# Kernel tuning notes

Measured on AMD Instinct MI355X. Metric: run time of the kernel, lower is better.

The kernel has to match this reference:

```python
import jax, jax.numpy as jnp
import numpy as np

N_NODES = 100_000
N_EDGES = 1_600_000
N_GRAPHS = 512
NF = 64        # n_node_feats
H1 = 128       # hidden width
H2 = 64        # dim_node_emb
DIM_OUT = 1
STEPS = 4      # set2set processing steps


def _lin(x, W, b):
    # torch Linear convention: y = x @ W.T + b, W: [out, in]
    return x @ W.T + b


def _gelu(x):
    return jax.nn.gelu(x, approximate=False)  # torch.nn.GELU default (erf)


def _lstm_cell(x, h, c, Wih, Whh, bih, bhh):
    g = x @ Wih.T + bih + h @ Whh.T + bhh
    i, f, gg, o = jnp.split(g, 4, axis=-1)  # torch gate order: i, f, g, o
    i, f, o = jax.nn.sigmoid(i), jax.nn.sigmoid(f), jax.nn.sigmoid(o)
    gg = jnp.tanh(gg)
    c = f * c + i * gg
    h = o * jnp.tanh(c)
    return h, c


def setup_inputs() -> dict:
    key = jax.random.key(0)
    ks = jax.random.split(key, 24)
    p = lambda k, shp: jax.random.normal(k, shp, dtype=jnp.float32) * 0.05
    inp = {
        "x": jax.random.normal(ks[0], (N_NODES, NF), dtype=jnp.float32),
        "edge_index": jax.random.randint(ks[1], (2, N_EDGES), 0, N_NODES, dtype=jnp.int32),
        "batch": jnp.sort(jax.random.randint(ks[2], (N_NODES,), 0, N_GRAPHS, dtype=jnp.int32)),
        "nfc_W": p(ks[3], (H1, NF)), "nfc_b": p(ks[4], (H1,)),
        "gc1_W": p(ks[5], (H1, H1)), "gc1_b": p(ks[6], (H1,)),
        "gc2_W": p(ks[7], (H2, H1)), "gc2_b": p(ks[8], (H2,)),
        "lstm0_Wih": p(ks[9], (4 * H2, 2 * H2)), "lstm0_Whh": p(ks[10], (4 * H2, H2)),
        "lstm0_bih": p(ks[11], (4 * H2,)), "lstm0_bhh": p(ks[12], (4 * H2,)),
        "lstm1_Wih": p(ks[13], (4 * H2, H2)), "lstm1_Whh": p(ks[14], (4 * H2, H2)),
        "lstm1_bih": p(ks[15], (4 * H2,)), "lstm1_bhh": p(ks[16], (4 * H2,)),
        "fc1_W": p(ks[17], (32, 2 * H2)), "fc1_b": p(ks[18], (32,)),
        "fc2_W": p(ks[19], (DIM_OUT, 32)), "fc2_b": p(ks[20], (DIM_OUT,)),
    }
    return inp


def _forward(x, edge_index, batch, nfc_W, nfc_b, gc1_W, gc1_b, gc2_W, gc2_b,
             lstm0_Wih, lstm0_Whh, lstm0_bih, lstm0_bhh,
             lstm1_Wih, lstm1_Whh, lstm1_bih, lstm1_bhh,
             fc1_W, fc1_b, fc2_W, fc2_b):
    src, dst = edge_index[0], edge_index[1]

    def gin_conv(h, W, b):
        # PyG GINConv, eps=0: lin((1+eps)*x + sum_{j in N(i)} x_j)
        agg = jax.ops.segment_sum(h[src], dst, num_segments=N_NODES)
        return _lin(h + agg, W, b)

    h = _gelu(_lin(x, nfc_W, nfc_b))
    h = _gelu(gin_conv(h, gc1_W, gc1_b))
    h = _gelu(gin_conv(h, gc2_W, gc2_b))
    # F.normalize(p=2, dim=1)
    h = h / jnp.maximum(jnp.linalg.norm(h, axis=1, keepdims=True), 1e-12)

    # Set2Set: 2-layer LSTM, 4 processing steps, scatter-softmax attention
    B = N_GRAPHS
    h0 = jnp.zeros((B, H2), jnp.float32); c0 = jnp.zeros((B, H2), jnp.float32)
    h1 = jnp.zeros((B, H2), jnp.float32); c1 = jnp.zeros((B, H2), jnp.float32)
    q_star = jnp.zeros((B, 2 * H2), jnp.float32)
    for _ in range(STEPS):
        h0, c0 = _lstm_cell(q_star, h0, c0, lstm0_Wih, lstm0_Whh, lstm0_bih, lstm0_bhh)
        h1, c1 = _lstm_cell(h0, h1, c1, lstm1_Wih, lstm1_Whh, lstm1_bih, lstm1_bhh)
        q = h1  # [B, H2]
        e = jnp.sum(h * q[batch], axis=-1, keepdims=True)  # [N, 1]
        m = jax.ops.segment_max(e, batch, num_segments=B)
        ex = jnp.exp(e - m[batch])
        s = jax.ops.segment_sum(ex, batch, num_segments=B)
        a = ex / (s[batch] + 1e-16)
        r = jax.ops.segment_sum(a * h, batch, num_segments=B)  # [B, H2]
        q_star = jnp.concatenate([q, r], axis=-1)

    z = _gelu(_lin(q_star, fc1_W, fc1_b))
    z = _lin(z, fc2_W, fc2_b)
    return z, h


def reference(x, edge_index, batch, nfc_W, nfc_b, gc1_W, gc1_b, gc2_W, gc2_b,
              lstm0_Wih, lstm0_Whh, lstm0_bih, lstm0_bhh,
              lstm1_Wih, lstm1_Whh, lstm1_bih, lstm1_bhh,
              fc1_W, fc1_b, fc2_W, fc2_b):
    return _forward(x, edge_index, batch, nfc_W, nfc_b, gc1_W, gc1_b, gc2_W, gc2_b,
                    lstm0_Wih, lstm0_Whh, lstm0_bih, lstm0_bhh,
                    lstm1_Wih, lstm1_Whh, lstm1_bih, lstm1_bhh,
                    fc1_W, fc1_b, fc2_W, fc2_b)
```

## Files before the change

### kernel.cpp

```cpp
#include <hip/hip_runtime.h>
#include <hip/hip_bf16.h>
#include <hip/hip_fp16.h>
#include <math.h>

constexpr int N  = 100000;
constexpr int E  = 1600000;
constexpr int NG = 512;
constexpr int NF = 64;
constexpr int H1 = 128;
constexpr int H2 = 64;

constexpr int BW   = 128;
constexpr int NB   = (N + BW - 1) / BW;
constexpr int CAP  = 2600;
constexpr int CHUNK = 4096;

constexpr int MAXN = 416;
constexpr int RST  = 68;

typedef __attribute__((ext_vector_type(8))) short short8;
typedef __attribute__((ext_vector_type(4))) float f32x4;

__device__ __forceinline__ float gelu_f(float x) {
    return 0.5f * x * (1.0f + erff(x * 0.70710678118654752f));
}
__device__ __forceinline__ float sigmoid_f(float x) {
    return 1.0f / (1.0f + expf(-x));
}
__device__ __forceinline__ float waveAllSum(float v) {
    #pragma unroll
    for (int m = 32; m; m >>= 1) v += __shfl_xor(v, m);
    return v;
}
__device__ __forceinline__ unsigned short f2bf(float x) {
    __hip_bfloat16 b = __float2bfloat16(x);
    return *reinterpret_cast<unsigned short*>(&b);
}
__device__ __forceinline__ float bf2f(unsigned short u) {
    return __uint_as_float(((unsigned int)u) << 16);
}
__device__ __forceinline__ float bf_lo(unsigned int u) { return __uint_as_float(u << 16); }
__device__ __forceinline__ float bf_hi(unsigned int u) { return __uint_as_float(u & 0xffff0000u); }

__device__ __forceinline__ void bfsplit(float v, unsigned short& hi, unsigned short& lo) {
    hi = f2bf(v);
    lo = f2bf(v - bf2f(hi));
}

__global__ __launch_bounds__(256) void setup_kernel(const int* __restrict__ batch,
                                                    const float* __restrict__ Wih0, const float* __restrict__ Whh0,
                                                    const float* __restrict__ bih0, const float* __restrict__ bhh0,
                                                    const float* __restrict__ Wih1, const float* __restrict__ Whh1,
                                                    const float* __restrict__ bih1, const float* __restrict__ bhh1,
                                                    float* __restrict__ WT0, float* __restrict__ WT1,
                                                    float* __restrict__ b0, float* __restrict__ b1,
                                                    int* __restrict__ bcursor, int* __restrict__ gstart) {
    int i = blockIdx.x * 256 + threadIdx.x;
    if (i < 192 * 256) {
        int k = i >> 8, j = i & 255;
        WT0[i] = (k < 128) ? Wih0[j * 128 + k] : Whh0[j * 64 + (k - 128)];
    }
    if (i < 128 * 256) {
        int k = i >> 8, j = i & 255;
        WT1[i] = (k < 64) ? Wih1[j * 64 + k] : Whh1[j * 64 + (k - 64)];
    }
    if (i < 256) { b0[i] = bih0[i] + bhh0[i]; b1[i] = bih1[i] + bhh1[i]; }
    if (i < NB) bcursor[i] = i * CAP;
    if (i <= NG) {
        if (i == NG) gstart[NG] = N;
        else {
            int lo = 0, hi = N;
            while (lo < hi) {
                int mid = (lo + hi) >> 1;
                if (batch[mid] < i) lo = mid + 1; else hi = mid;
            }
            gstart[i] = lo;
        }
    }
}

__global__ __launch_bounds__(256) void bin_scatter_kernel(const int* __restrict__ ei,
                                                          int* __restrict__ bcursor,
                                                          int* __restrict__ pairs) {
    __shared__ int hist[NB];
    __shared__ int start_s[NB];
    __shared__ int lcur[NB];
    int tid = threadIdx.x;
    int e0 = blockIdx.x * CHUNK;
    for (int b = tid; b < NB; b += 256) hist[b] = 0;
    __syncthreads();
    #pragma unroll 4
    for (int k = 0; k < CHUNK / 256; ++k) {
        int e = e0 + k * 256 + tid;
        if (e < E) atomicAdd(&hist[ei[E + e] >> 7], 1);
    }
    __syncthreads();
    for (int b = tid; b < NB; b += 256) {
        if (hist[b]) start_s[b] = atomicAdd(&bcursor[b], hist[b]);
        lcur[b] = 0;
    }
    __syncthreads();
    #pragma unroll 4
    for (int k = 0; k < CHUNK / 256; ++k) {
        int e = e0 + k * 256 + tid;
        if (e < E) {
            int d = ei[E + e];
            int s = ei[e];
            int b = d >> 7;
            int pos = start_s[b] + atomicAdd(&lcur[b], 1);
            if (pos < (b + 1) * CAP) pairs[pos] = (s << 7) | (d & 127);
        }
    }
}

__global__ __launch_bounds__(256) void csr_bucket_kernel(const int* __restrict__ pairs,
                                                         const int* __restrict__ bcursor,
                                                         int* __restrict__ srcs,
                                                         int2* __restrict__ nrange) {
    __shared__ int cnt_l[BW];
    __shared__ int cur_l[BW];
    __shared__ int wt[2];
    int b = blockIdx.x;
    int tid = threadIdx.x;
    int base = b * CAP;
    int cnt = bcursor[b] - base;
    if (cnt > CAP) cnt = CAP;
    if (tid < BW) cnt_l[tid] = 0;
    __syncthreads();
    for (int i = tid; i < cnt; i += 256) {
        atomicAdd(&cnt_l[pairs[base + i] & 127], 1);
    }
    __syncthreads();
    if (tid < BW) {
        int v = cnt_l[tid];
        int lane = tid & 63, w = tid >> 6;
        int incl = v;
        #pragma unroll
        for (int off = 1; off < 64; off <<= 1) {
            int t = __shfl_up(incl, off);
            if (lane >= off) incl += t;
        }
        if (lane == 63) wt[w] = incl;
        __syncthreads();
        int excl = (w ? wt[0] : 0) + incl - v;
        int node = b * BW + tid;
        if (node < N) nrange[node] = make_int2(base + excl, base + excl + v);
        cur_l[tid] = excl;
    } else {
        __syncthreads();
    }
    __syncthreads();
    for (int i = tid; i < cnt; i += 256) {
        int p = pairs[base + i];
        int pos = atomicAdd(&cur_l[p & 127], 1);
        srcs[base + pos] = p >> 7;
    }
}

template <int ID, int OD>
__global__ __launch_bounds__(256) void lin_mfma_kernel(const float* __restrict__ in,
                                                       const float* __restrict__ W,
                                                       const float* __restrict__ bias,
                                                       unsigned short* __restrict__ out_bf, int nrows) {
    constexpr int KC = 32;
    constexpr int NCH = ID / KC;
    constexpr int AST = 40;
    constexpr int NCT = OD / 16;
    constexpr int LDSU = 2 * 128 * AST + 2 * OD * AST;
    __shared__ __align__(16) unsigned short lds[LDSU];
    unsigned short* Ahi = lds;
    unsigned short* Alo = lds + 128 * AST;
    unsigned short* Whi = lds + 2 * 128 * AST;
    unsigned short* Wlo = lds + 2 * 128 * AST + OD * AST;

    int tid = threadIdx.x;
    int w = tid >> 6, lane = tid & 63;
    int m15 = lane & 15, quad = lane >> 4;
    int nb = blockIdx.x * 128;

    f32x4 acc[2][NCT];
    #pragma unroll
    for (int rt = 0; rt < 2; ++rt)
        #pragma unroll
        for (int ct = 0; ct < NCT; ++ct) acc[rt][ct] = (f32x4)0.f;

    for (int c = 0; c < NCH; ++c) {
        int kb = c * KC;
        #pragma unroll
        for (int it = 0; it < 4; ++it) {
            int f4 = it * 256 + tid;
            int row = f4 >> 3, kq = (f4 & 7) * 4;
            float4 v = make_float4(0.f, 0.f, 0.f, 0.f);
            if (nb + row < nrows) v = *(const float4*)&in[(size_t)(nb + row) * ID + kb + kq];
            unsigned short h0, h1, h2, h3, l0, l1, l2, l3;
            bfsplit(v.x, h0, l0); bfsplit(v.y, h1, l1);
            bfsplit(v.z, h2, l2); bfsplit(v.w, h3, l3);
            uint2 uh, ul;
            uh.x = (unsigned int)h0 | ((unsigned int)h1 << 16);
            uh.y = (unsigned int)h2 | ((unsigned int)h3 << 16);
            ul.x = (unsigned int)l0 | ((unsigned int)l1 << 16);
            ul.y = (unsigned int)l2 | ((unsigned int)l3 << 16);
            *(uint2*)&Ahi[row * AST + kq] = uh;
            *(uint2*)&Alo[row * AST + kq] = ul;
        }
        #pragma unroll
        for (int it = 0; it < OD / 32; ++it) {
            int f4 = it * 256 + tid;
            int o = f4 >> 3, kq = (f4 & 7) * 4;
            float4 v = *(const float4*)&W[(size_t)o * ID + kb + kq];
            unsigned short h0, h1, h2, h3, l0, l1, l2, l3;
            bfsplit(v.x, h0, l0); bfsplit(v.y, h1, l1);
            bfsplit(v.z, h2, l2); bfsplit(v.w, h3, l3);
            uint2 uh, ul;
            uh.x = (unsigned int)h0 | ((unsigned int)h1 << 16);
            uh.y = (unsigned int)h2 | ((unsigned int)h3 << 16);
            ul.x = (unsigned int)l0 | ((unsigned int)l1 << 16);
            ul.y = (unsigned int)l2 | ((unsigned int)l3 << 16);
            *(uint2*)&Whi[o * AST + kq] = uh;
            *(uint2*)&Wlo[o * AST + kq] = ul;
        }
        __syncthreads();

        short8 ah0 = *(const short8*)&Ahi[(w * 32 + m15) * AST + quad * 8];
        short8 ah1 = *(const short8*)&Ahi[(w * 32 + 16 + m15) * AST + quad * 8];
        short8 al0 = *(const short8*)&Alo[(w * 32 + m15) * AST + quad * 8];
        short8 al1 = *(const short8*)&Alo[(w * 32 + 16 + m15) * AST + quad * 8];
        #pragma unroll
        for (int ct = 0; ct < NCT; ++ct) {
            short8 bh = *(const short8*)&Whi[(ct * 16 + m15) * AST + quad * 8];
            short8 bl = *(const short8*)&Wlo[(ct * 16 + m15) * AST + quad * 8];
            acc[0][ct] = __builtin_amdgcn_mfma_f32_16x16x32_bf16(ah0, bh, acc[0][ct], 0, 0, 0);
            acc[0][ct] = __builtin_amdgcn_mfma_f32_16x16x32_bf16(ah0, bl, acc[0][ct], 0, 0, 0);
            acc[0][ct] = __builtin_amdgcn_mfma_f32_16x16x32_bf16(al0, bh, acc[0][ct], 0, 0, 0);
            acc[1][ct] = __builtin_amdgcn_mfma_f32_16x16x32_bf16(ah1, bh, acc[1][ct], 0, 0, 0);
            acc[1][ct] = __builtin_amdgcn_mfma_f32_16x16x32_bf16(ah1, bl, acc[1][ct], 0, 0, 0);
            acc[1][ct] = __builtin_amdgcn_mfma_f32_16x16x32_bf16(al1, bh, acc[1][ct], 0, 0, 0);
        }
        __syncthreads();
    }

    float bcol[NCT];
    #pragma unroll
    for (int ct = 0; ct < NCT; ++ct) bcol[ct] = bias[ct * 16 + m15];

    constexpr int EPS = OD + 8;
    unsigned short* ep = lds;
    #pragma unroll
    for (int rt = 0; rt < 2; ++rt)
        #pragma unroll
        for (int ct = 0; ct < NCT; ++ct)
            #pragma unroll
            for (int r = 0; r < 4; ++r) {
                int rl = w * 32 + rt * 16 + quad * 4 + r;
                float v = gelu_f(acc[rt][ct][r] + bcol[ct]);
                ep[rl * EPS + ct * 16 + m15] = f2bf(v);
            }
    __syncthreads();
    constexpr int U4 = 128 * OD / 8;
    for (int i = tid; i < U4; i += 256) {
        int row = i / (OD / 8);
        int off = (i % (OD / 8)) * 8;
        int grow = nb + row;
        if (grow < nrows) {
            uint4 v = *(const uint4*)&ep[row * EPS + off];
            *(uint4*)(out_bf + (size_t)grow * OD + off) = v;
        }
    }
}

__global__ __launch_bounds__(256) void agg_kernel(const uint2* __restrict__ hb2,
                                                  const int2* __restrict__ nrange,
                                                  const int* __restrict__ srcs,
                                                  uint4* __restrict__ utab) {
    int wave = threadIdx.x >> 6, lane = threadIdx.x & 63;
    int half = lane >> 5, hl = lane & 31;
    int n = blockIdx.x * 4 + wave;
    if (n >= N) return;
    int2 rng = nrange[n];
    int s0 = rng.x, deg = rng.y - rng.x;
    int m1 = deg < 64 ? deg : 64;
    int pre = (lane < m1) ? srcs[s0 + lane] : 0;
    float a0 = 0.f, a1 = 0.f, a2 = 0.f, a3 = 0.f;
    int t = 0;
    for (; t + 8 <= m1; t += 8) {
        int i0 = __shfl(pre, t + half);
        int i1 = __shfl(pre, t + 2 + half);
        int i2 = __shfl(pre, t + 4 + half);
        int i3 = __shfl(pre, t + 6 + half);
        uint2 u0 = hb2[(size_t)i0 * 32 + hl];
        uint2 u1 = hb2[(size_t)i1 * 32 + hl];
        uint2 u2 = hb2[(size_t)i2 * 32 + hl];
        uint2 u3 = hb2[(size_t)i3 * 32 + hl];
        a0 += bf_lo(u0.x); a1 += bf_hi(u0.x); a2 += bf_lo(u0.y); a3 += bf_hi(u0.y);
        a0 += bf_lo(u1.x); a1 += bf_hi(u1.x); a2 += bf_lo(u1.y); a3 += bf_hi(u1.y);
        a0 += bf_lo(u2.x); a1 += bf_hi(u2.x); a2 += bf_lo(u2.y); a3 += bf_hi(u2.y);
        a0 += bf_lo(u3.x); a1 += bf_hi(u3.x); a2 += bf_lo(u3.y); a3 += bf_hi(u3.y);
    }
    for (; t < m1; t += 2) {
        int idx = t + half;
        int idc = idx < m1 ? idx : 0;
        int s = __shfl(pre, idc);
        if (idx < m1) {
            uint2 u = hb2[(size_t)s * 32 + hl];
            a0 += bf_lo(u.x); a1 += bf_hi(u.x); a2 += bf_lo(u.y); a3 += bf_hi(u.y);
        }
    }
    for (int j = 64 + half; j < deg; j += 2) {
        int s = srcs[s0 + j];
        uint2 u = hb2[(size_t)s * 32 + hl];
        a0 += bf_lo(u.x); a1 += bf_hi(u.x); a2 += bf_lo(u.y); a3 += bf_hi(u.y);
    }
    a0 += __shfl_down(a0, 32);
    a1 += __shfl_down(a1, 32);
    a2 += __shfl_down(a2, 32);
    a3 += __shfl_down(a3, 32);
    if (half == 0) {
        uint2 u = hb2[(size_t)n * 32 + hl];
        a0 += bf_lo(u.x); a1 += bf_hi(u.x); a2 += bf_lo(u.y); a3 += bf_hi(u.y);
        unsigned short h0, h1, h2, h3, l0, l1, l2, l3;
        bfsplit(a0, h0, l0); bfsplit(a1, h1, l1);
        bfsplit(a2, h2, l2); bfsplit(a3, h3, l3);
        uint4 o;
        o.x = (unsigned int)h0 | ((unsigned int)h1 << 16);
        o.y = (unsigned int)h2 | ((unsigned int)h3 << 16);
        o.z = (unsigned int)l0 | ((unsigned int)l1 << 16);
        o.w = (unsigned int)l2 | ((unsigned int)l3 << 16);
        utab[(size_t)n * 32 + hl] = o;
    }
}

__global__ __launch_bounds__(256) void lin2_fused_kernel(const uint4* __restrict__ in4,
                                                         const float* __restrict__ W1,
                                                         const float* __restrict__ b1,
                                                         const float* __restrict__ W2,
                                                         unsigned short* __restrict__ y2,
                                                         int nrows) {
    constexpr int AST = 40;
    __shared__ __align__(16) unsigned short lds[4 * 128 * AST];
    unsigned short* Ahi = lds;
    unsigned short* Alo = lds + 128 * AST;
    unsigned short* Whi = lds + 2 * 128 * AST;
    unsigned short* Wlo = lds + 3 * 128 * AST;

    int tid = threadIdx.x;
    int w = tid >> 6, lane = tid & 63;
    int m15 = lane & 15, quad = lane >> 4;
    int nb = blockIdx.x * 128;

    f32x4 acc[2][8];
    #pragma unroll
    for (int rt = 0; rt < 2; ++rt)
        #pragma unroll
        for (int ct = 0; ct < 8; ++ct) acc[rt][ct] = (f32x4)0.f;

    for (int c = 0; c < 4; ++c) {
        #pragma unroll
        for (int it = 0; it < 4; ++it) {
            int i = it * 256 + tid;
            int row = i >> 3, grp = i & 7;
            uint4 u = make_uint4(0u, 0u, 0u, 0u);
            if (nb + row < nrows) u = in4[(size_t)(nb + row) * 32 + c * 8 + grp];
            *(uint2*)&Ahi[row * AST + grp * 4] = make_uint2(u.x, u.y);
            *(uint2*)&Alo[row * AST + grp * 4] = make_uint2(u.z, u.w);
        }
        #pragma unroll
        for (int it = 0; it < 4; ++it) {
            int f4 = it * 256 + tid;
            int o = f4 >> 3, kq = (f4 & 7) * 4;
            float4 v = *(const float4*)&W1[(size_t)o * 128 + c * 32 + kq];
            unsigned short h0, h1, h2, h3, l0, l1, l2, l3;
            bfsplit(v.x, h0, l0); bfsplit(v.y, h1, l1);
            bfsplit(v.z, h2, l2); bfsplit(v.w, h3, l3);
            uint2 uh, ul;
            uh.x = (unsigned int)h0 | ((unsigned int)h1 << 16);
            uh.y = (unsigned int)h2 | ((unsigned int)h3 << 16);
            ul.x = (unsigned int)l0 | ((unsigned int)l1 << 16);
            ul.y = (unsigned int)l2 | ((unsigned int)l3 << 16);
            *(uint2*)&Whi[o * AST + kq] = uh;
            *(uint2*)&Wlo[o * AST + kq] = ul;
        }
        __syncthreads();
        short8 ah0 = *(const short8*)&Ahi[(w * 32 + m15) * AST + quad * 8];
        short8 ah1 = *(const short8*)&Ahi[(w * 32 + 16 + m15) * AST + quad * 8];
        short8 al0 = *(const short8*)&Alo[(w * 32 + m15) * AST + quad * 8];
        short8 al1 = *(const short8*)&Alo[(w * 32 + 16 + m15) * AST + quad * 8];
        #pragma unroll
        for (int ct = 0; ct < 8; ++ct) {
            short8 bh = *(const short8*)&Whi[(ct * 16 + m15) * AST + quad * 8];
            short8 bl = *(const short8*)&Wlo[(ct * 16 + m15) * AST + quad * 8];
            acc[0][ct] = __builtin_amdgcn_mfma_f32_16x16x32_bf16(ah0, bh, acc[0][ct], 0, 0, 0);
            acc[0][ct] = __builtin_amdgcn_mfma_f32_16x16x32_bf16(ah0, bl, acc[0][ct], 0, 0, 0);
            acc[0][ct] = __builtin_amdgcn_mfma_f32_16x16x32_bf16(al0, bh, acc[0][ct], 0, 0, 0);
            acc[1][ct] = __builtin_amdgcn_mfma_f32_16x16x32_bf16(ah1, bh, acc[1][ct], 0, 0, 0);
            acc[1][ct] = __builtin_amdgcn_mfma_f32_16x16x32_bf16(ah1, bl, acc[1][ct], 0, 0, 0);
            acc[1][ct] = __builtin_amdgcn_mfma_f32_16x16x32_bf16(al1, bh, acc[1][ct], 0, 0, 0);
        }
        __syncthreads();
    }

    #pragma unroll
    for (int ct = 0; ct < 8; ++ct) {
        float bc = b1[ct * 16 + m15];
        #pragma unroll
        for (int rt = 0; rt < 2; ++rt)
            #pragma unroll
            for (int r = 0; r < 4; ++r)
                acc[rt][ct][r] = gelu_f(acc[rt][ct][r] + bc);
    }

    f32x4 acc2[2][4];
    #pragma unroll
    for (int rt = 0; rt < 2; ++rt)
        #pragma unroll
        for (int ct = 0; ct < 4; ++ct) acc2[rt][ct] = (f32x4)0.f;

    for (int c2 = 0; c2 < 4; ++c2) {
        __syncthreads();
        #pragma unroll
        for (int rt = 0; rt < 2; ++rt)
            #pragma unroll
            for (int cc = 0; cc < 2; ++cc) {
                int ct = c2 * 2 + cc;
                #pragma unroll
                for (int r = 0; r < 4; ++r) {
                    int node = w * 32 + rt * 16 + quad * 4 + r;
                    unsigned short hi, lo;
                    bfsplit(acc[rt][ct][r], hi, lo);
                    Ahi[node * AST + cc * 16 + m15] = hi;
                    Alo[node * AST + cc * 16 + m15] = lo;
                }
            }
        #pragma unroll
        for (int it = 0; it < 2; ++it) {
            int f4 = it * 256 + tid;
            int o = f4 >> 3, kq = (f4 & 7) * 4;
            float4 v = *(const float4*)&W2[(size_t)o * 128 + c2 * 32 + kq];
            unsigned short h0, h1, h2, h3, l0, l1, l2, l3;
            bfsplit(v.x, h0, l0); bfsplit(v.y, h1, l1);
            bfsplit(v.z, h2, l2); bfsplit(v.w, h3, l3);
            uint2 uh, ul;
            uh.x = (unsigned int)h0 | ((unsigned int)h1 << 16);
            uh.y = (unsigned int)h2 | ((unsigned int)h3 << 16);
            ul.x = (unsigned int)l0 | ((unsigned int)l1 << 16);
            ul.y = (unsigned int)l2 | ((unsigned int)l3 << 16);
            *(uint2*)&Whi[o * AST + kq] = uh;
            *(uint2*)&Wlo[o * AST + kq] = ul;
        }
        __syncthreads();
        short8 ah0 = *(const short8*)&Ahi[(w * 32 + m15) * AST + quad * 8];
        short8 ah1 = *(const short8*)&Ahi[(w * 32 + 16 + m15) * AST + quad * 8];
        short8 al0 = *(const short8*)&Alo[(w * 32 + m15) * AST + quad * 8];
        short8 al1 = *(const short8*)&Alo[(w * 32 + 16 + m15) * AST + quad * 8];
        #pragma unroll
        for (int ct = 0; ct < 4; ++ct) {
            short8 bh = *(const short8*)&Whi[(ct * 16 + m15) * AST + quad * 8];
            short8 bl = *(const short8*)&Wlo[(ct * 16 + m15) * AST + quad * 8];
            acc2[0][ct] = __builtin_amdgcn_mfma_f32_16x16x32_bf16(ah0, bh, acc2[0][ct], 0, 0, 0);
            acc2[0][ct] = __builtin_amdgcn_mfma_f32_16x16x32_bf16(ah0, bl, acc2[0][ct], 0, 0, 0);
            acc2[0][ct] = __builtin_amdgcn_mfma_f32_16x16x32_bf16(al0, bh, acc2[0][ct], 0, 0, 0);
            acc2[1][ct] = __builtin_amdgcn_mfma_f32_16x16x32_bf16(ah1, bh, acc2[1][ct], 0, 0, 0);
            acc2[1][ct] = __builtin_amdgcn_mfma_f32_16x16x32_bf16(ah1, bl, acc2[1][ct], 0, 0, 0);
            acc2[1][ct] = __builtin_amdgcn_mfma_f32_16x16x32_bf16(al1, bh, acc2[1][ct], 0, 0, 0);
        }
    }
    __syncthreads();

    constexpr int EPS = 72;
    unsigned short* ep = lds;
    #pragma unroll
    for (int rt = 0; rt < 2; ++rt)
        #pragma unroll
        for (int ct = 0; ct < 4; ++ct)
            #pragma unroll
            for (int r = 0; r < 4; ++r) {
                int rl = w * 32 + rt * 16 + quad * 4 + r;
                __half hv = __float2half(acc2[rt][ct][r]);
                ep[rl * EPS + ct * 16 + m15] = *reinterpret_cast<unsigned short*>(&hv);
            }
    __syncthreads();
    for (int i = tid; i < 1024; i += 256) {
        int row = i >> 3, off = (i & 7) * 8;
        int grow = nb + row;
        if (grow < nrows)
            *(uint4*)(y2 + (size_t)grow * 64 + off) = *(const uint4*)&ep[row * EPS + off];
    }
}

__global__ __launch_bounds__(256) void agg2_norm_kernel(const uint2* __restrict__ y2,
                                                        const int2* __restrict__ nrange,
                                                        const int* __restrict__ srcs,
                                                        const float* __restrict__ b2,
                                                        float* __restrict__ hn) {
    int wave = threadIdx.x >> 6, lane = threadIdx.x & 63;
    int qw = lane >> 4, ql = lane & 15;
    int n = blockIdx.x * 4 + wave;
    if (n >= N) return;
    int2 rng = nrange[n];
    int s0 = rng.x, deg = rng.y - rng.x;
    int m1 = deg < 64 ? deg : 64;
    int pre = (lane < m1) ? srcs[s0 + lane] : 0;
    float a0 = 0.f, a1 = 0.f, a2 = 0.f, a3 = 0.f;
    auto addu = [&](uint2 u) {
        float2 f01 = __half22float2(*reinterpret_cast<__half2*>(&u.x));
        float2 f23 = __half22float2(*reinterpret_cast<__half2*>(&u.y));
        a0 += f01.x; a1 += f01.y; a2 += f23.x; a3 += f23.y;
    };
    int t = 0;
    for (; t + 8 <= m1; t += 8) {
        int i0 = __shfl(pre, t + qw);
        int i1 = __shfl(pre, t + 4 + qw);
        uint2 u0 = y2[(size_t)i0 * 16 + ql];
        uint2 u1 = y2[(size_t)i1 * 16 + ql];
        addu(u0); addu(u1);
    }
    for (; t < m1; t += 4) {
        int idx = t + qw;
        int s = __shfl(pre, idx < m1 ? idx : 0);
        if (idx < m1) addu(y2[(size_t)s * 16 + ql]);
    }
    for (int j = 64 + qw; j < deg; j += 4) addu(y2[(size_t)srcs[s0 + j] * 16 + ql]);
    a0 += __shfl_down(a0, 32); a1 += __shfl_down(a1, 32);
    a2 += __shfl_down(a2, 32); a3 += __shfl_down(a3, 32);
    a0 += __shfl_down(a0, 16); a1 += __shfl_down(a1, 16);
    a2 += __shfl_down(a2, 16); a3 += __shfl_down(a3, 16);
    if (qw == 0) {
        addu(y2[(size_t)n * 16 + ql]);
        float4 bv = *(const float4*)&b2[ql * 4];
        float v0 = gelu_f(a0 + bv.x), v1 = gelu_f(a1 + bv.y);
        float v2 = gelu_f(a2 + bv.z), v3 = gelu_f(a3 + bv.w);
        float ss = v0 * v0 + v1 * v1 + v2 * v2 + v3 * v3;
        #pragma unroll
        for (int mm = 1; mm < 16; mm <<= 1) ss += __shfl_xor(ss, mm);
        float d = fmaxf(sqrtf(ss), 1e-12f);
        *(float4*)&hn[(size_t)n * 64 + ql * 4] = make_float4(v0 / d, v1 / d, v2 / d, v3 / d);
    }
}

__global__ __launch_bounds__(256) void set2set_kernel(const float* __restrict__ hn,
                                                      const int* __restrict__ gstart,
                                                      const float* __restrict__ WT0, const float* __restrict__ b0,
                                                      const float* __restrict__ WT1, const float* __restrict__ b1,
                                                      float* __restrict__ qstar_out) {
    __shared__ __align__(16) unsigned short hL[MAXN * RST];
    __shared__ float av[MAXN];
    __shared__ __align__(16) float xc0[192];
    __shared__ __align__(16) float xc1[128];
    __shared__ __align__(16) float gates[256];
    __shared__ float c0v[H2], c1v[H2];
    __shared__ float red[4];
    __shared__ float rp[4][H2];
    __shared__ float sp[4];

    int g = blockIdx.x;
    int tid = threadIdx.x, w = tid >> 6, lane = tid & 63;
    int s0 = gstart[g], s1 = gstart[g + 1];
    int cnt = s1 - s0;
    int cL = cnt < MAXN ? cnt : MAXN;
    const float* hq = xc1 + 64;

    for (int idx = tid; idx < cL * 16; idx += 256) {
        int n = idx >> 4, p4 = idx & 15;
        float4 v = *(const float4*)&hn[(size_t)(s0 + n) * 64 + p4 * 4];
        uint2 u;
        u.x = (unsigned int)f2bf(v.x) | ((unsigned int)f2bf(v.y) << 16);
        u.y = (unsigned int)f2bf(v.z) | ((unsigned int)f2bf(v.w) << 16);
        *(uint2*)&hL[n * RST + p4 * 4] = u;
    }
    if (tid < 192) xc0[tid] = 0.f;
    if (tid < 128) xc1[tid] = 0.f;
    if (tid < H2) { c0v[tid] = 0.f; c1v[tid] = 0.f; }
    float b0v = b0[tid], b1v = b1[tid];
    __syncthreads();

    for (int step = 0; step < 4; ++step) {
        {
            float a0 = 0.f, a1 = 0.f, a2 = 0.f, a3 = 0.f;
            #pragma unroll 8
            for (int k = 0; k < 192; k += 4) {
                a0 += xc0[k]     * WT0[(k)     * 256 + tid];
                a1 += xc0[k + 1] * WT0[(k + 1) * 256 + tid];
                a2 += xc0[k + 2] * WT0[(k + 2) * 256 + tid];
                a3 += xc0[k + 3] * WT0[(k + 3) * 256 + tid];
            }
            gates[tid] = (a0 + a1) + (a2 + a3) + b0v;
        }
        __syncthreads();
        if (tid < H2) {
            float ii = sigmoid_f(gates[tid]), ff = sigmoid_f(gates[H2 + tid]);
            float gg = tanhf(gates[2 * H2 + tid]), oo = sigmoid_f(gates[3 * H2 + tid]);
            float c = ff * c0v[tid] + ii * gg;
            float h = oo * tanhf(c);
            c0v[tid] = c; xc0[128 + tid] = h; xc1[tid] = h;
        }
        __syncthreads();
        {
            float a0 = 0.f, a1 = 0.f, a2 = 0.f, a3 = 0.f;
            #pragma unroll 8
            for (int k = 0; k < 128; k += 4) {
                a0 += xc1[k]     * WT1[(k)     * 256 + tid];
                a1 += xc1[k + 1] * WT1[(k + 1) * 256 + tid];
                a2 += xc1[k + 2] * WT1[(k + 2) * 256 + tid];
                a3 += xc1[k + 3] * WT1[(k + 3) * 256 + tid];
            }
            gates[tid] = (a0 + a1) + (a2 + a3) + b1v;
        }
        __syncthreads();
        if (tid < H2) {
            float ii = sigmoid_f(gates[tid]), ff = sigmoid_f(gates[H2 + tid]);
            float gg = tanhf(gates[2 * H2 + tid]), oo = sigmoid_f(gates[3 * H2 + tid]);
            float c = ff * c1v[tid] + ii * gg;
            float h = oo * tanhf(c);
            c1v[tid] = c; xc1[64 + tid] = h;
        }
        __syncthreads();

        float lm = -INFINITY;
        for (int i = tid; i < cnt; i += 256) {
            float e = 0.f;
            if (i < MAXN) {
                const uint2* row = (const uint2*)&hL[i * RST];
                #pragma unroll
                for (int p4 = 0; p4 < 16; ++p4) {
                    uint2 u = row[p4];
                    e += bf_lo(u.x) * hq[p4 * 4 + 0];
                    e += bf_hi(u.x) * hq[p4 * 4 + 1];
                    e += bf_lo(u.y) * hq[p4 * 4 + 2];
                    e += bf_hi(u.y) * hq[p4 * 4 + 3];
                }
                av[i] = e;
            } else {
                for (int f = 0; f < 64; ++f) e += hn[(size_t)(s0 + i) * 64 + f] * hq[f];
            }
            lm = fmaxf(lm, e);
        }
        #pragma unroll
        for (int mm = 32; mm; mm >>= 1) lm = fmaxf(lm, __shfl_xor(lm, mm));
        if (lane == 0) red[w] = lm;
        __syncthreads();
        float m = fmaxf(fmaxf(red[0], red[1]), fmaxf(red[2], red[3]));

        float ps = 0.f;
        for (int i = tid; i < cnt; i += 256) {
            float e;
            if (i < MAXN) e = av[i];
            else {
                e = 0.f;
                for (int f = 0; f < 64; ++f) e += hn[(size_t)(s0 + i) * 64 + f] * hq[f];
            }
            float p = expf(e - m);
            ps += p;
            if (i < MAXN) av[i] = p;
        }
        ps = waveAllSum(ps);
        if (lane == 0) sp[w] = ps;
        __syncthreads();
        float s = sp[0] + sp[1] + sp[2] + sp[3];

        float racc = 0.f;
        for (int i = w; i < cL; i += 4) {
            unsigned short hv = hL[i * RST + lane];
            racc += av[i] * bf2f(hv);
        }
        float qf = hq[lane];
        for (int n = MAXN + w; n < cnt; n += 4) {
            float v = hn[(size_t)(s0 + n) * 64 + lane];
            float e = waveAllSum(v * qf);
            float p = expf(e - m);
            racc += p * v;
        }
        rp[w][lane] = racc;
        __syncthreads();
        if (tid < H2) {
            float r = 0.f;
            if (cnt > 0) {
                r = (rp[0][tid] + rp[1][tid] + rp[2][tid] + rp[3][tid]) / (s + 1e-16f);
            }
            xc0[tid] = xc1[64 + tid];
            xc0[H2 + tid] = r;
        }
        __syncthreads();
    }
    if (tid < 2 * H2) qstar_out[g * 2 * H2 + tid] = xc0[tid];
}

__global__ __launch_bounds__(256) void fcout_kernel(const float* __restrict__ q_star,
                                                    const float* __restrict__ W1, const float* __restrict__ b1,
                                                    const float* __restrict__ W2, const float* __restrict__ b2,
                                                    float* __restrict__ z) {
    __shared__ float W1l[32 * 128];
    __shared__ float b1l[32], W2l[32];
    int tid = threadIdx.x;
    for (int i = tid; i < 32 * 128; i += 256) W1l[i] = W1[i];
    if (tid < 32) { b1l[tid] = b1[tid]; W2l[tid] = W2[tid]; }
    __syncthreads();
    int g = blockIdx.x * 256 + tid;
    float acc[32];
    #pragma unroll
    for (int j = 0; j < 32; ++j) acc[j] = b1l[j];
    for (int k = 0; k < 128; ++k) {
        float qv = q_star[g * 128 + k];
        #pragma unroll
        for (int j = 0; j < 32; ++j) acc[j] += qv * W1l[j * 128 + k];
    }
    float zv = b2[0];
    #pragma unroll
    for (int j = 0; j < 32; ++j) zv += gelu_f(acc[j]) * W2l[j];
    z[g] = zv;
}

extern "C" void kernel_launch(void* const* d_in, const int* in_sizes, int n_in,
                              void* d_out, int out_size, void* d_ws, size_t ws_size,
                              hipStream_t stream) {
    const float* x       = (const float*)d_in[0];
    const int*   ei      = (const int*)d_in[1];
    const int*   batch   = (const int*)d_in[2];
    const float* nfc_W   = (const float*)d_in[3];
    const float* nfc_b   = (const float*)d_in[4];
    const float* gc1_W   = (const float*)d_in[5];
    const float* gc1_b   = (const float*)d_in[6];
    const float* gc2_W   = (const float*)d_in[7];
    const float* gc2_b   = (const float*)d_in[8];
    const float* l0_Wih  = (const float*)d_in[9];
    const float* l0_Whh  = (const float*)d_in[10];
    const float* l0_bih  = (const float*)d_in[11];
    const float* l0_bhh  = (const float*)d_in[12];
    const float* l1_Wih  = (const float*)d_in[13];
    const float* l1_Whh  = (const float*)d_in[14];
    const float* l1_bih  = (const float*)d_in[15];
    const float* l1_bhh  = (const float*)d_in[16];
    const float* fc1_W   = (const float*)d_in[17];
    const float* fc1_b   = (const float*)d_in[18];
    const float* fc2_W   = (const float*)d_in[19];
    const float* fc2_b   = (const float*)d_in[20];

    float* out = (float*)d_out;
    float* hn_out = out + NG;

    char* p = (char*)d_ws;
    auto take = [&](size_t bytes) {
        char* r = p;
        p += (bytes + 255) & ~size_t(255);
        return r;
    };
    float*          sbuf  = (float*)take((size_t)N * H1 * 4);
    unsigned short* hbbuf = (unsigned short*)take((size_t)N * H1 * 2);
    int*   srcs   = (int*)take((size_t)NB * CAP * 4);
    int2*  nrange = (int2*)take((size_t)N * 8);
    int*   bcursor= (int*)take((size_t)NB * 4);
    int*   gstart = (int*)take((size_t)(NG + 1) * 4);
    float* qstar  = (float*)take((size_t)NG * 2 * H2 * 4);
    float* WT0    = (float*)take((size_t)192 * 256 * 4);
    float* WT1    = (float*)take((size_t)128 * 256 * 4);
    float* b0     = (float*)take((size_t)256 * 4);
    float* b1     = (float*)take((size_t)256 * 4);

    int* pairs = (int*)sbuf;

    setup_kernel<<<192, 256, 0, stream>>>(batch, l0_Wih, l0_Whh, l0_bih, l0_bhh,
                                          l1_Wih, l1_Whh, l1_bih, l1_bhh,
                                          WT0, WT1, b0, b1, bcursor, gstart);

    bin_scatter_kernel<<<(E + CHUNK - 1) / CHUNK, 256, 0, stream>>>(ei, bcursor, pairs);
    csr_bucket_kernel<<<NB, 256, 0, stream>>>(pairs, bcursor, srcs, nrange);

    int mfmaGrid = (N + 127) / 128;
    lin_mfma_kernel<NF, H1><<<mfmaGrid, 256, 0, stream>>>(x, nfc_W, nfc_b, hbbuf, N);
    agg_kernel<<<(N + 3) / 4, 256, 0, stream>>>((const uint2*)hbbuf, nrange, srcs, (uint4*)sbuf);
    lin2_fused_kernel<<<mfmaGrid, 256, 0, stream>>>((const uint4*)sbuf, gc1_W, gc1_b, gc2_W,
                                                    hbbuf, N);
    agg2_norm_kernel<<<(N + 3) / 4, 256, 0, stream>>>((const uint2*)hbbuf, nrange, srcs,
                                                      gc2_b, hn_out);

    set2set_kernel<<<NG, 256, 0, stream>>>(hn_out, gstart, WT0, b0, WT1, b1, qstar);

    fcout_kernel<<<2, 256, 0, stream>>>(qstar, fc1_W, fc1_b, fc2_W, fc2_b, out);
}
```

Before: 468.8 us.

## Pre-split GIN weights into MFMA fragment layout and drop block syncs in lin2

The setup kernel now converts gc1/gc2 weights once into bf16 hi/lo pairs stored in MFMA-fragment order. The fused two-layer linear kernel loads these fragments and its input rows straight from global memory into registers, and each wave uses a private LDS slice, so block-wide __syncthreads are gone. This removes the per-block weight conversion and the shared-LDS staging barriers. In exchange it relies on L1/L2 caching of repeated weight loads and on manual lgkmcnt waits, and it adds a launch bound of 3 blocks per SM.

Result: no change. 470.2 us (+0.3%).

```diff
diff --git a/kernel.cpp b/kernel.cpp
--- a/kernel.cpp
+++ b/kernel.cpp
@@ -52,8 +52,10 @@
                                                     const float* __restrict__ bih0, const float* __restrict__ bhh0,
                                                     const float* __restrict__ Wih1, const float* __restrict__ Whh1,
                                                     const float* __restrict__ bih1, const float* __restrict__ bhh1,
+                                                    const float* __restrict__ gc1W, const float* __restrict__ gc2W,
                                                     float* __restrict__ WT0, float* __restrict__ WT1,
                                                     float* __restrict__ b0, float* __restrict__ b1,
+                                                    unsigned short* __restrict__ W1F, unsigned short* __restrict__ W2F,
                                                     int* __restrict__ bcursor, int* __restrict__ gstart) {
     int i = blockIdx.x * 256 + threadIdx.x;
     if (i < 192 * 256) {
@@ -63,6 +65,24 @@
     if (i < 128 * 256) {
         int k = i >> 8, j = i & 255;
         WT1[i] = (k < 64) ? Wih1[j * 64 + k] : Whh1[j * 64 + (k - 64)];
+    }
+    if (i < 16384) {
+        int f = i >> 9, r = i & 511, l = r >> 3, j = r & 7;
+        int c = f >> 3, ct = f & 7;
+        int o = ct * 16 + (l & 15), k = c * 32 + (l >> 4) * 8 + j;
+        unsigned short hi, lo;
+        bfsplit(gc1W[o * 128 + k], hi, lo);
+        W1F[f * 1024 + r] = hi;
+        W1F[f * 1024 + 512 + r] = lo;
+    }
+    if (i < 8192) {
+        int f = i >> 9, r = i & 511, l = r >> 3, j = r & 7;
+        int c2 = f >> 2, ct2 = f & 3;
+        int o = ct2 * 16 + (l & 15), k = c2 * 32 + (l >> 4) * 8 + j;
+        unsigned short hi, lo;
+        bfsplit(gc2W[o * 128 + k], hi, lo);
+        W2F[f * 1024 + r] = hi;
+        W2F[f * 1024 + 512 + r] = lo;
     }
     if (i < 256) { b0[i] = bih0[i] + bhh0[i]; b1[i] = bih1[i] + bhh1[i]; }
     if (i < NB) bcursor[i] = i * CAP;
@@ -329,23 +349,27 @@
     }
 }
 
-__global__ __launch_bounds__(256) void lin2_fused_kernel(const uint4* __restrict__ in4,
-                                                         const float* __restrict__ W1,
-                                                         const float* __restrict__ b1,
-                                                         const float* __restrict__ W2,
-                                                         unsigned short* __restrict__ y2,
-                                                         int nrows) {
-    constexpr int AST = 40;
-    __shared__ __align__(16) unsigned short lds[4 * 128 * AST];
-    unsigned short* Ahi = lds;
-    unsigned short* Alo = lds + 128 * AST;
-    unsigned short* Whi = lds + 2 * 128 * AST;
-    unsigned short* Wlo = lds + 3 * 128 * AST;
-
-    int tid = threadIdx.x;
-    int w = tid >> 6, lane = tid & 63;
+__global__ __launch_bounds__(256, 3) void lin2_fused_kernel(const uint4* __restrict__ in4,
+                                                            const uint4* __restrict__ W1F,
+                                                            const float* __restrict__ b1,
+                                                            const uint4* __restrict__ W2F,
+                                                            unsigned short* __restrict__ y2,
+                                                            int nrows) {
+    constexpr int AST2 = 40;
+    __shared__ __align__(16) unsigned short lds[4 * 2560];
+    union U8 { uint4 u; short8 s; };
+    int tid = threadIdx.x, w = tid >> 6, lane = tid & 63;
     int m15 = lane & 15, quad = lane >> 4;
-    int nb = blockIdx.x * 128;
+    unsigned short* myL = lds + w * 2560;
+    int rowbase = blockIdx.x * 128 + w * 32;
+    int r0 = rowbase + m15;      if (r0 >= nrows) r0 = nrows - 1;
+    int r1 = rowbase + 16 + m15; if (r1 >= nrows) r1 = nrows - 1;
+    const uint4* a0p = in4 + (size_t)r0 * 32 + quad * 2;
+    const uint4* a1p = in4 + (size_t)r1 * 32 + quad * 2;
+
+    float bc[8];
+    #pragma unroll
+    for (int ct = 0; ct < 8; ++ct) bc[ct] = b1[ct * 16 + m15];
 
     f32x4 acc[2][8];
     #pragma unroll
@@ -353,41 +377,21 @@
         #pragma unroll
         for (int ct = 0; ct < 8; ++ct) acc[rt][ct] = (f32x4)0.f;
 
+    #pragma unroll
     for (int c = 0; c < 4; ++c) {
-        #pragma unroll
-        for (int it = 0; it < 4; ++it) {
-            int i = it * 256 + tid;
-            int row = i >> 3, grp = i & 7;
-            uint4 u = make_uint4(0u, 0u, 0u, 0u);
-            if (nb + row < nrows) u = in4[(size_t)(nb + row) * 32 + c * 8 + grp];
-            *(uint2*)&Ahi[row * AST + grp * 4] = make_uint2(u.x, u.y);
-            *(uint2*)&Alo[row * AST + grp * 4] = make_uint2(u.z, u.w);
-        }
-        #pragma unroll
-        for (int it = 0; it < 4; ++it) {
-            int f4 = it * 256 + tid;
-            int o = f4 >> 3, kq = (f4 & 7) * 4;
-            float4 v = *(const float4*)&W1[(size_t)o * 128 + c * 32 + kq];
-            unsigned short h0, h1, h2, h3, l0, l1, l2, l3;
-            bfsplit(v.x, h0, l0); bfsplit(v.y, h1, l1);
-            bfsplit(v.z, h2, l2); bfsplit(v.w, h3, l3);
-            uint2 uh, ul;
-            uh.x = (unsigned int)h0 | ((unsigned int)h1 << 16);
-            uh.y = (unsigned int)h2 | ((unsigned int)h3 << 16);
-            ul.x = (unsigned int)l0 | ((unsigned int)l1 << 16);
-            ul.y = (unsigned int)l2 | ((unsigned int)l3 << 16);
-            *(uint2*)&Whi[o * AST + kq] = uh;
-            *(uint2*)&Wlo[o * AST + kq] = ul;
-        }
-        __syncthreads();
-        short8 ah0 = *(const short8*)&Ahi[(w * 32 + m15) * AST + quad * 8];
-        short8 ah1 = *(const short8*)&Ahi[(w * 32 + 16 + m15) * AST + quad * 8];
-        short8 al0 = *(const short8*)&Alo[(w * 32 + m15) * AST + quad * 8];
-        short8 al1 = *(const short8*)&Alo[(w * 32 + 16 + m15) * AST + quad * 8];
+        uint4 u00 = a0p[c * 8], u01 = a0p[c * 8 + 1];
+        uint4 u10 = a1p[c * 8], u11 = a1p[c * 8 + 1];
+        U8 t;
+        t.u = make_uint4(u00.x, u00.y, u01.x, u01.y); short8 ah0 = t.s;
+        t.u = make_uint4(u00.z, u00.w, u01.z, u01.w); short8 al0 = t.s;
+        t.u = make_uint4(u10.x, u10.y, u11.x, u11.y); short8 ah1 = t.s;
+        t.u = make_uint4(u10.z, u10.w, u11.z, u11.w); short8 al1 = t.s;
         #pragma unroll
         for (int ct = 0; ct < 8; ++ct) {
-            short8 bh = *(const short8*)&Whi[(ct * 16 + m15) * AST + quad * 8];
-            short8 bl = *(const short8*)&Wlo[(ct * 16 + m15) * AST + quad * 8];
+            U8 th, tl;
+            th.u = W1F[(c * 8 + ct) * 128 + lane];
+            tl.u = W1F[(c * 8 + ct) * 128 + 64 + lane];
+            short8 bh = th.s, bl = tl.s;
             acc[0][ct] = __builtin_amdgcn_mfma_f32_16x16x32_bf16(ah0, bh, acc[0][ct], 0, 0, 0);
             acc[0][ct] = __builtin_amdgcn_mfma_f32_16x16x32_bf16(ah0, bl, acc[0][ct], 0, 0, 0);
             acc[0][ct] = __builtin_amdgcn_mfma_f32_16x16x32_bf16(al0, bh, acc[0][ct], 0, 0, 0);
@@ -395,27 +399,26 @@
             acc[1][ct] = __builtin_amdgcn_mfma_f32_16x16x32_bf16(ah1, bl, acc[1][ct], 0, 0, 0);
             acc[1][ct] = __builtin_amdgcn_mfma_f32_16x16x32_bf16(al1, bh, acc[1][ct], 0, 0, 0);
         }
-        __syncthreads();
-    }
-
-    #pragma unroll
-    for (int ct = 0; ct < 8; ++ct) {
-        float bc = b1[ct * 16 + m15];
+    }
+
+    #pragma unroll
+    for (int ct = 0; ct < 8; ++ct)
         #pragma unroll
         for (int rt = 0; rt < 2; ++rt)
             #pragma unroll
             for (int r = 0; r < 4; ++r)
-                acc[rt][ct][r] = gelu_f(acc[rt][ct][r] + bc);
-    }
-
+                acc[rt][ct][r] = gelu_f(acc[rt][ct][r] + bc[ct]);
+
+    unsigned short* Ahi2 = myL;
+    unsigned short* Alo2 = myL + 32 * AST2;
     f32x4 acc2[2][4];
     #pragma unroll
     for (int rt = 0; rt < 2; ++rt)
         #pragma unroll
         for (int ct = 0; ct < 4; ++ct) acc2[rt][ct] = (f32x4)0.f;
 
+    #pragma unroll
     for (int c2 = 0; c2 < 4; ++c2) {
-        __syncthreads();
         #pragma unroll
         for (int rt = 0; rt < 2; ++rt)
             #pragma unroll
@@ -423,66 +426,52 @@
                 int ct = c2 * 2 + cc;
                 #pragma unroll
                 for (int r = 0; r < 4; ++r) {
-                    int node = w * 32 + rt * 16 + quad * 4 + r;
+                    int node = rt * 16 + quad * 4 + r;
                     unsigned short hi, lo;
                     bfsplit(acc[rt][ct][r], hi, lo);
-                    Ahi[node * AST + cc * 16 + m15] = hi;
-                    Alo[node * AST + cc * 16 + m15] = lo;
+                    Ahi2[node * AST2 + cc * 16 + m15] = hi;
+                    Alo2[node * AST2 + cc * 16 + m15] = lo;
                 }
             }
-        #pragma unroll
-        for (int it = 0; it < 2; ++it) {
-            int f4 = it * 256 + tid;
-            int o = f4 >> 3, kq = (f4 & 7) * 4;
-            float4 v = *(const float4*)&W2[(size_t)o * 128 + c2 * 32 + kq];
-            unsigned short h0, h1, h2, h3, l0, l1, l2, l3;
-            bfsplit(v.x, h0, l0); bfsplit(v.y, h1, l1);
-            bfsplit(v.z, h2, l2); bfsplit(v.w, h3, l3);
-            uint2 uh, ul;
-            uh.x = (unsigned int)h0 | ((unsigned int)h1 << 16);
-            uh.y = (unsigned int)h2 | ((unsigned int)h3 << 16);
-            ul.x = (unsigned int)l0 | ((unsigned int)l1 << 16);
-            ul.y = (unsigned int)l2 | ((unsigned int)l3 << 16);
-            *(uint2*)&Whi[o * AST + kq] = uh;
-            *(uint2*)&Wlo[o * AST + kq] = ul;
-        }
-        __syncthreads();
-        short8 ah0 = *(const short8*)&Ahi[(w * 32 + m15) * AST + quad * 8];
-        short8 ah1 = *(const short8*)&Ahi[(w * 32 + 16 + m15) * AST + quad * 8];
-        short8 al0 = *(const short8*)&Alo[(w * 32 + m15) * AST + quad * 8];
-        short8 al1 = *(const short8*)&Alo[(w * 32 + 16 + m15) * AST + quad * 8];
-        #pragma unroll
-        for (int ct = 0; ct < 4; ++ct) {
-            short8 bh = *(const short8*)&Whi[(ct * 16 + m15) * AST + quad * 8];
-            short8 bl = *(const short8*)&Wlo[(ct * 16 + m15) * AST + quad * 8];
-            acc2[0][ct] = __builtin_amdgcn_mfma_f32_16x16x32_bf16(ah0, bh, acc2[0][ct], 0, 0, 0);
-            acc2[0][ct] = __builtin_amdgcn_mfma_f32_16x16x32_bf16(ah0, bl, acc2[0][ct], 0, 0, 0);
-            acc2[0][ct] = __builtin_amdgcn_mfma_f32_16x16x32_bf16(al0, bh, acc2[0][ct], 0, 0, 0);
-            acc2[1][ct] = __builtin_amdgcn_mfma_f32_16x16x32_bf16(ah1, bh, acc2[1][ct], 0, 0, 0);
-            acc2[1][ct] = __builtin_amdgcn_mfma_f32_16x16x32_bf16(ah1, bl, acc2[1][ct], 0, 0, 0);
-            acc2[1][ct] = __builtin_amdgcn_mfma_f32_16x16x32_bf16(al1, bh, acc2[1][ct], 0, 0, 0);
-        }
-    }
-    __syncthreads();
-
-    constexpr int EPS = 72;
-    unsigned short* ep = lds;
+        asm volatile("s_waitcnt lgkmcnt(0)" ::: "memory");
+        short8 ah0 = *(const short8*)&Ahi2[m15 * AST2 + quad * 8];
+        short8 ah1 = *(const short8*)&Ahi2[(16 + m15) * AST2 + quad * 8];
+        short8 al0 = *(const short8*)&Alo2[m15 * AST2 + quad * 8];
+        short8 al1 = *(const short8*)&Alo2[(16 + m15) * AST2 + quad * 8];
+        #pragma unroll
+        for (int ct2 = 0; ct2 < 4; ++ct2) {
+            U8 th, tl;
+            th.u = W2F[(c2 * 4 + ct2) * 128 + lane];
+            tl.u = W2F[(c2 * 4 + ct2) * 128 + 64 + lane];
+            short8 bh = th.s, bl = tl.s;
+            acc2[0][ct2] = __builtin_amdgcn_mfma_f32_16x16x32_bf16(ah0, bh, acc2[0][ct2], 0, 0, 0);
+            acc2[0][ct2] = __builtin_amdgcn_mfma_f32_16x16x32_bf16(ah0, bl, acc2[0][ct2], 0, 0, 0);
+            acc2[0][ct2] = __builtin_amdgcn_mfma_f32_16x16x32_bf16(al0, bh, acc2[0][ct2], 0, 0, 0);
+            acc2[1][ct2] = __builtin_amdgcn_mfma_f32_16x16x32_bf16(ah1, bh, acc2[1][ct2], 0, 0, 0);
+            acc2[1][ct2] = __builtin_amdgcn_mfma_f32_16x16x32_bf16(ah1, bl, acc2[1][ct2], 0, 0, 0);
+            acc2[1][ct2] = __builtin_amdgcn_mfma_f32_16x16x32_bf16(al1, bh, acc2[1][ct2], 0, 0, 0);
+        }
+    }
+
+    unsigned short* ep = myL;
     #pragma unroll
     for (int rt = 0; rt < 2; ++rt)
         #pragma unroll
-        for (int ct = 0; ct < 4; ++ct)
+        for (int ct2 = 0; ct2 < 4; ++ct2)
             #pragma unroll
             for (int r = 0; r < 4; ++r) {
-                int rl = w * 32 + rt * 16 + quad * 4 + r;
-                __half hv = __float2half(acc2[rt][ct][r]);
-                ep[rl * EPS + ct * 16 + m15] = *reinterpret_cast<unsigned short*>(&hv);
-            }
-    __syncthreads();
-    for (int i = tid; i < 1024; i += 256) {
-        int row = i >> 3, off = (i & 7) * 8;
-        int grow = nb + row;
+                int node = rt * 16 + quad * 4 + r;
+                __half hv = __float2half(acc2[rt][ct2][r]);
+                ep[node * 72 + ct2 * 16 + m15] = *reinterpret_cast<unsigned short*>(&hv);
+            }
+    asm volatile("s_waitcnt lgkmcnt(0)" ::: "memory");
+    #pragma unroll
+    for (int it = 0; it < 4; ++it) {
+        int idx = it * 64 + lane;
+        int rowl = idx >> 3, off = (idx & 7) * 8;
+        int grow = rowbase + rowl;
         if (grow < nrows)
-            *(uint4*)(y2 + (size_t)grow * 64 + off) = *(const uint4*)&ep[row * EPS + off];
+            *(uint4*)(y2 + (size_t)grow * 64 + off) = *(const uint4*)&ep[rowl * 72 + off];
     }
 }
 
@@ -753,12 +742,15 @@
     float* WT1    = (float*)take((size_t)128 * 256 * 4);
     float* b0     = (float*)take((size_t)256 * 4);
     float* b1     = (float*)take((size_t)256 * 4);
+    unsigned short* W1F = (unsigned short*)take((size_t)32 * 1024 * 2);
+    unsigned short* W2F = (unsigned short*)take((size_t)16 * 1024 * 2);
 
     int* pairs = (int*)sbuf;
 
     setup_kernel<<<192, 256, 0, stream>>>(batch, l0_Wih, l0_Whh, l0_bih, l0_bhh,
                                           l1_Wih, l1_Whh, l1_bih, l1_bhh,
-                                          WT0, WT1, b0, b1, bcursor, gstart);
+                                          gc1_W, gc2_W,
+                                          WT0, WT1, b0, b1, W1F, W2F, bcursor, gstart);
 
     bin_scatter_kernel<<<(E + CHUNK - 1) / CHUNK, 256, 0, stream>>>(ei, bcursor, pairs);
     csr_bucket_kernel<<<NB, 256, 0, stream>>>(pairs, bcursor, srcs, nrange);
@@ -766,8 +758,8 @@
     int mfmaGrid = (N + 127) / 128;
     lin_mfma_kernel<NF, H1><<<mfmaGrid, 256, 0, stream>>>(x, nfc_W, nfc_b, hbbuf, N);
     agg_kernel<<<(N + 3) / 4, 256, 0, stream>>>((const uint2*)hbbuf, nrange, srcs, (uint4*)sbuf);
-    lin2_fused_kernel<<<mfmaGrid, 256, 0, stream>>>((const uint4*)sbuf, gc1_W, gc1_b, gc2_W,
-                                                    hbbuf, N);
+    lin2_fused_kernel<<<mfmaGrid, 256, 0, stream>>>((const uint4*)sbuf, (const uint4*)W1F, gc1_b,
+                                                    (const uint4*)W2F, hbbuf, N);
     agg2_norm_kernel<<<(N + 3) / 4, 256, 0, stream>>>((const uint2*)hbbuf, nrange, srcs,
                                                       gc2_b, hn_out);
 
```
